# Kernel tuning notes

Measured on AMD Instinct MI355X. Metric: run time of the kernel, lower is better.

The kernel has to match this reference:

```python
import jax, jax.numpy as jnp
import numpy as np
import itertools

N, F, R, O, OUT = 131072, 32, 256, 5, 100
K = 9  # 2*exp_param + 1 with exp_param=4


def setup_inputs() -> dict:
    key = jax.random.key(0)
    k1, k2, k3 = jax.random.split(key, 3)
    # binary features -> get_route(x)==1 -> categorical rule path
    x = jax.random.randint(k1, (N, F), 0, 2).astype(jnp.float32)
    # first R combinations of O feature indices out of F (itertools order, as in __init__)
    combs = np.array(list(itertools.islice(itertools.combinations(range(F), O), R)), dtype=np.int32)
    comb_space = jax.random.normal(k2, (O, R), dtype=jnp.float32)
    w_out = jax.random.normal(k3, (OUT, R), dtype=jnp.float32) * 0.05
    b_out = jnp.zeros((OUT,), jnp.float32)
    return {"x": x, "comb_space": comb_space, "w_out": w_out, "b_out": b_out,
            "comb_idx": jnp.asarray(combs)}


def reference(x, comb_space, w_out, b_out, comb_idx):
    # Fused version of the per-rule Python loop:
    # gather all rule feature subsets at once: [N, R, O]
    gathered = x[:, comb_idx]
    # per-rule dot product with its parameter vector comb_space[:, r]
    scores = jnp.einsum('nro,or->nr', gathered, comb_space)  # [N, R]
    # polyClip activation: clamp(s^k, -1, 1)
    comb_pred = jnp.clip(scores ** K, -1.0, 1.0)
    # dropout p=0.1 is identity in eval mode
    attn = jax.nn.softmax(comb_pred, axis=1)                 # [N, R]
    out = attn @ w_out.T + b_out                             # [N, OUT]
    return jax.nn.log_softmax(out, axis=1)
```

## Files before the change

### kernel.cpp

```cpp
#include <hip/hip_runtime.h>

typedef unsigned short u16;
typedef _Float16 f16;
typedef __attribute__((ext_vector_type(2))) __fp16 hf16x2;
typedef __attribute__((ext_vector_type(4))) _Float16 f16x4;
typedef __attribute__((ext_vector_type(8))) _Float16 f16x8;
typedef __attribute__((ext_vector_type(4))) float f32x4;

#define N_ROWS 131072
#define FDIM 32
#define RDIM 256
#define ODIM 5
#define NOUT 100
#define JT 7
#define WAVES 8
#define ROWS_PER_BLOCK (WAVES * 16)
#define NBLOCKS (N_ROWS / ROWS_PER_BLOCK)

#define MF_SLOTS 1024
#define WF_SLOTS (JT * 8 * 64)
#define TAB_SLOTS (MF_SLOTS + WF_SLOTS)

#define CSCALE 1.04156363f
#define CLIP2  1.44269504f

typedef const __attribute__((address_space(1))) void gvoid;
typedef __attribute__((address_space(3))) void lvoid;

__device__ __forceinline__ u16 f2h_bits(float f) {
    f16 h = (f16)f;
    union { f16 h; u16 u; } v; v.h = h;
    return v.u;
}

__global__ void build_tabs(const float* __restrict__ cs, const float* __restrict__ w,
                           const int* __restrict__ ci, u16* __restrict__ tabs) {
    int t = blockIdx.x * 512 + threadIdx.x;
    if (t >= TAB_SLOTS) return;
    u16 vals[8];
    if (t < MF_SLOTS) {
        int l = t & 63, rt = t >> 6;
        int r = rt * 16 + (l & 15);
        int kbase = (l >> 4) * 8;
        int idx0 = ci[r * ODIM + 0], idx1 = ci[r * ODIM + 1], idx2 = ci[r * ODIM + 2];
        int idx3 = ci[r * ODIM + 3], idx4 = ci[r * ODIM + 4];
#pragma unroll
        for (int e = 0; e < 8; ++e) {
            int k = kbase + e;
            float v = 0.f;
            if (idx0 == k) v = cs[0 * RDIM + r];
            if (idx1 == k) v = cs[1 * RDIM + r];
            if (idx2 == k) v = cs[2 * RDIM + r];
            if (idx3 == k) v = cs[3 * RDIM + r];
            if (idx4 == k) v = cs[4 * RDIM + r];
            vals[e] = f2h_bits(v * CSCALE);
        }
    } else {
        int s = t - MF_SLOTS;
        int l = s & 63, ft = s >> 6;
        int jt = ft >> 3, rtp = ft & 7;
        int j = jt * 16 + (l & 15);
        if (j < NOUT) {
            const float* wp = w + (size_t)j * RDIM + rtp * 32 + (l >> 4) * 4;
            float4 va = *(const float4*)wp;
            float4 vb = *(const float4*)(wp + 16);
            vals[0] = f2h_bits(va.x); vals[1] = f2h_bits(va.y);
            vals[2] = f2h_bits(va.z); vals[3] = f2h_bits(va.w);
            vals[4] = f2h_bits(vb.x); vals[5] = f2h_bits(vb.y);
            vals[6] = f2h_bits(vb.z); vals[7] = f2h_bits(vb.w);
        } else {
            u16 fill = (j == NOUT) ? f2h_bits(1.0f) : (u16)0;
#pragma unroll
            for (int e = 0; e < 8; ++e) vals[e] = fill;
        }
    }
    *(uint4*)(tabs + (size_t)t * 8) = *(const uint4*)vals;
}

__device__ __forceinline__ f16x4 elemop(f32x4 cc) {
    float ev[4];
#pragma unroll
    for (int i = 0; i < 4; ++i) {
        float s = cc[i];
        float s2 = s * s, s4 = s2 * s2, s8 = s4 * s4;
        float p = __builtin_amdgcn_fmed3f(s8 * s, -CLIP2, CLIP2);
        float e;
        asm("v_exp_f32 %0, %1" : "=v"(e) : "v"(p));
        ev[i] = e;
    }
    union { hf16x2 h; unsigned u; } lo, hi;
    lo.h = __builtin_amdgcn_cvt_pkrtz(ev[0], ev[1]);
    hi.h = __builtin_amdgcn_cvt_pkrtz(ev[2], ev[3]);
    union { unsigned u[2]; f16x4 v; } r;
    r.u[0] = lo.u; r.u[1] = hi.u;
    return r.v;
}

__global__ __launch_bounds__(WAVES * 64, 2) void hornet_main(
    const float* __restrict__ x, const u16* __restrict__ tabs,
    const float* __restrict__ b_out, float* __restrict__ out)
{
    __shared__ __align__(16) u16 tab[TAB_SLOTS * 8];

    const int tid = threadIdx.x;
    const int lane = tid & 63;
    const int wid = tid >> 6;
    const int c15 = lane & 15, g = lane >> 4;

    const int rowb0 = blockIdx.x * ROWS_PER_BLOCK + wid * 16;
    const float* xp0 = x + (size_t)(rowb0 + c15) * FDIM + g * 8;
    float4 x0a = ((const float4*)xp0)[0];
    float4 x0b = ((const float4*)xp0)[1];

#pragma unroll
    for (int i = 0; i < 9; ++i) {
        const u16* gp = tabs + (size_t)(tid + i * 512) * 8;
        u16* lp = tab + (size_t)(wid * 64 + i * 512) * 8;
        __builtin_amdgcn_global_load_lds((gvoid*)gp, (lvoid*)lp, 16, 0, 0);
    }

    f16x8 a1;
    a1[0] = (f16)x0a.x; a1[1] = (f16)x0a.y; a1[2] = (f16)x0a.z; a1[3] = (f16)x0a.w;
    a1[4] = (f16)x0b.x; a1[5] = (f16)x0b.y; a1[6] = (f16)x0b.z; a1[7] = (f16)x0b.w;

    __syncthreads();

    const f16x8* mfv = (const f16x8*)tab;
    const f16x8* wfv = (const f16x8*)(tab + MF_SLOTS * 8);

    f32x4 acc[JT];
#pragma unroll
    for (int jt = 0; jt < JT; ++jt) acc[jt] = (f32x4){0.f, 0.f, 0.f, 0.f};

    f16x8 b1a = mfv[lane];
    f16x8 b1b = mfv[64 + lane];

#pragma unroll 1
    for (int rtp = 0; rtp < 8; ++rtp) {
        f16x8 ca = b1a, cb = b1b;
        int nrtp = (rtp + 1) & 7;
        b1a = mfv[(2 * nrtp) * 64 + lane];
        b1b = mfv[(2 * nrtp + 1) * 64 + lane];

        const f32x4 z = {0.f, 0.f, 0.f, 0.f};
        __builtin_amdgcn_s_setprio(1);
        f32x4 cca = __builtin_amdgcn_mfma_f32_16x16x32_f16(ca, a1, z, 0, 0, 0);
        f32x4 ccb = __builtin_amdgcn_mfma_f32_16x16x32_f16(cb, a1, z, 0, 0, 0);
        __builtin_amdgcn_s_setprio(0);

        f16x4 a2lo = elemop(cca);
        f16x4 a2hi = elemop(ccb);

        const f16x8* wrow = wfv + rtp * 64 + lane;
        __builtin_amdgcn_s_setprio(1);
#pragma unroll
        for (int jt = 0; jt < JT; ++jt) {
            f16x8 b2 = wrow[jt * 8 * 64];
            f16x4 b2lo = __builtin_shufflevector(b2, b2, 0, 1, 2, 3);
            f16x4 b2hi = __builtin_shufflevector(b2, b2, 4, 5, 6, 7);
            acc[jt] = __builtin_amdgcn_mfma_f32_16x16x16f16(a2lo, b2lo, acc[jt], 0, 0, 0);
            acc[jt] = __builtin_amdgcn_mfma_f32_16x16x16f16(a2hi, b2hi, acc[jt], 0, 0, 0);
        }
        __builtin_amdgcn_s_setprio(0);
    }

    float bv[JT];
#pragma unroll
    for (int jt = 0; jt < JT; ++jt) {
        int j = jt * 16 + c15;
        bv[jt] = (j < NOUT) ? b_out[j] : 0.f;
    }

    float rin[4];
#pragma unroll
    for (int i = 0; i < 4; ++i)
        rin[i] = __builtin_amdgcn_rcpf(__shfl(acc[6][i], g * 16 + 4, 64));
    const bool v6 = (c15 < 4);
#pragma unroll
    for (int i = 0; i < 4; ++i) {
        float lg[JT];
        float se = 0.f;
#pragma unroll
        for (int jt = 0; jt < 6; ++jt) {
            lg[jt] = fmaf(acc[jt][i], rin[i], bv[jt]);
            se += __expf(lg[jt]);
        }
        lg[6] = fmaf(acc[6][i], rin[i], bv[6]);
        se += v6 ? __expf(lg[6]) : 0.f;
#pragma unroll
        for (int m = 1; m <= 8; m <<= 1) se += __shfl_xor(se, m, 64);
        float lse = __logf(se);
        int row = rowb0 + g * 4 + i;
        float* op = out + (size_t)row * NOUT;
#pragma unroll
        for (int jt = 0; jt < 6; ++jt) op[jt * 16 + c15] = lg[jt] - lse;
        if (v6) op[96 + c15] = lg[6] - lse;
    }
}

extern "C" void kernel_launch(void* const* d_in, const int* in_sizes, int n_in,
                              void* d_out, int out_size, void* d_ws, size_t ws_size,
                              hipStream_t stream) {
    const float* x  = (const float*)d_in[0];
    const float* cs = (const float*)d_in[1];
    const float* w  = (const float*)d_in[2];
    const float* b  = (const float*)d_in[3];
    const int*   ci = (const int*)d_in[4];

    u16* tabs = (u16*)d_ws;

    hipLaunchKernelGGL(build_tabs, dim3(9), dim3(512), 0, stream, cs, w, ci, tabs);
    hipLaunchKernelGGL(hornet_main, dim3(NBLOCKS), dim3(WAVES * 64), 0, stream,
                       x, tabs, b, (float*)d_out);
}
```

Baseline: 31.76 us.

## Read weight tables from global cache, shrink blocks, packed fp16 activation math

Removes the per-block LDS staging of the 72KB weight/mapping tables and reads them directly from global memory (relying on L1/L2 caching). The block shrinks to 4 waves with occupancy target 8. The pow9/clip/exp activation is rewritten as packed fp16 ops with v_exp_f16 instead of fp32 per-element math. This avoids the LDS fill and barrier and the LDS capacity limit on occupancy, at the cost of more global/cache traffic per MFMA operand load and reduced precision in the activation (fp16 overflow of s^9 is clipped).

```diff
diff --git a/kernel.cpp b/kernel.cpp
--- a/kernel.cpp
+++ b/kernel.cpp
@@ -1,6 +1,7 @@
 #include <hip/hip_runtime.h>
 
 typedef unsigned short u16;
+typedef unsigned int u32;
 typedef _Float16 f16;
 typedef __attribute__((ext_vector_type(2))) __fp16 hf16x2;
 typedef __attribute__((ext_vector_type(4))) _Float16 f16x4;
@@ -13,7 +14,7 @@
 #define ODIM 5
 #define NOUT 100
 #define JT 7
-#define WAVES 8
+#define WAVES 4
 #define ROWS_PER_BLOCK (WAVES * 16)
 #define NBLOCKS (N_ROWS / ROWS_PER_BLOCK)
 
@@ -22,10 +23,6 @@
 #define TAB_SLOTS (MF_SLOTS + WF_SLOTS)
 
 #define CSCALE 1.04156363f
-#define CLIP2  1.44269504f
-
-typedef const __attribute__((address_space(1))) void gvoid;
-typedef __attribute__((address_space(3))) void lvoid;
 
 __device__ __forceinline__ u16 f2h_bits(float f) {
     f16 h = (f16)f;
@@ -35,7 +32,7 @@
 
 __global__ void build_tabs(const float* __restrict__ cs, const float* __restrict__ w,
                            const int* __restrict__ ci, u16* __restrict__ tabs) {
-    int t = blockIdx.x * 512 + threadIdx.x;
+    int t = blockIdx.x * 256 + threadIdx.x;
     if (t >= TAB_SLOTS) return;
     u16 vals[8];
     if (t < MF_SLOTS) {
@@ -77,31 +74,35 @@
     *(uint4*)(tabs + (size_t)t * 8) = *(const uint4*)vals;
 }
 
-__device__ __forceinline__ f16x4 elemop(f32x4 cc) {
-    float ev[4];
-#pragma unroll
-    for (int i = 0; i < 4; ++i) {
-        float s = cc[i];
-        float s2 = s * s, s4 = s2 * s2, s8 = s4 * s4;
-        float p = __builtin_amdgcn_fmed3f(s8 * s, -CLIP2, CLIP2);
-        float e;
-        asm("v_exp_f32 %0, %1" : "=v"(e) : "v"(p));
-        ev[i] = e;
-    }
-    union { hf16x2 h; unsigned u; } lo, hi;
-    lo.h = __builtin_amdgcn_cvt_pkrtz(ev[0], ev[1]);
-    hi.h = __builtin_amdgcn_cvt_pkrtz(ev[2], ev[3]);
-    union { unsigned u[2]; f16x4 v; } r;
-    r.u[0] = lo.u; r.u[1] = hi.u;
+__device__ __forceinline__ u32 pk_pow9_clip_exp(u32 h, u32 cpos, u32 cneg, u32 psel) {
+    u32 h2, h4, h8, p, phi, elo, ehi, r;
+    asm("v_pk_mul_f16 %0, %1, %1" : "=v"(h2) : "v"(h));
+    asm("v_pk_mul_f16 %0, %1, %1" : "=v"(h4) : "v"(h2));
+    asm("v_pk_mul_f16 %0, %1, %1" : "=v"(h8) : "v"(h4));
+    asm("v_pk_mul_f16 %0, %1, %2" : "=v"(p) : "v"(h8), "v"(h));
+    asm("v_pk_max_f16 %0, %1, %2" : "=v"(p) : "v"(p), "v"(cneg));
+    asm("v_pk_min_f16 %0, %1, %2" : "=v"(p) : "v"(p), "v"(cpos));
+    asm("v_lshrrev_b32 %0, 16, %1" : "=v"(phi) : "v"(p));
+    asm("v_exp_f16 %0, %1" : "=v"(elo) : "v"(p));
+    asm("v_exp_f16 %0, %1" : "=v"(ehi) : "v"(phi));
+    asm("v_perm_b32 %0, %1, %2, %3" : "=v"(r) : "v"(ehi), "v"(elo), "v"(psel));
+    return r;
+}
+
+__device__ __forceinline__ f16x4 elemop(f32x4 cc, u32 cpos, u32 cneg, u32 psel) {
+    union { hf16x2 h; u32 u; } h01, h23;
+    h01.h = __builtin_amdgcn_cvt_pkrtz(cc[0], cc[1]);
+    h23.h = __builtin_amdgcn_cvt_pkrtz(cc[2], cc[3]);
+    union { u32 u[2]; f16x4 v; } r;
+    r.u[0] = pk_pow9_clip_exp(h01.u, cpos, cneg, psel);
+    r.u[1] = pk_pow9_clip_exp(h23.u, cpos, cneg, psel);
     return r.v;
 }
 
-__global__ __launch_bounds__(WAVES * 64, 2) void hornet_main(
+__global__ __launch_bounds__(WAVES * 64, 8) void hornet_main(
     const float* __restrict__ x, const u16* __restrict__ tabs,
     const float* __restrict__ b_out, float* __restrict__ out)
 {
-    __shared__ __align__(16) u16 tab[TAB_SLOTS * 8];
-
     const int tid = threadIdx.x;
     const int lane = tid & 63;
     const int wid = tid >> 6;
@@ -112,21 +113,16 @@
     float4 x0a = ((const float4*)xp0)[0];
     float4 x0b = ((const float4*)xp0)[1];
 
-#pragma unroll
-    for (int i = 0; i < 9; ++i) {
-        const u16* gp = tabs + (size_t)(tid + i * 512) * 8;
-        u16* lp = tab + (size_t)(wid * 64 + i * 512) * 8;
-        __builtin_amdgcn_global_load_lds((gvoid*)gp, (lvoid*)lp, 16, 0, 0);
-    }
-
     f16x8 a1;
     a1[0] = (f16)x0a.x; a1[1] = (f16)x0a.y; a1[2] = (f16)x0a.z; a1[3] = (f16)x0a.w;
     a1[4] = (f16)x0b.x; a1[5] = (f16)x0b.y; a1[6] = (f16)x0b.z; a1[7] = (f16)x0b.w;
 
-    __syncthreads();
-
-    const f16x8* mfv = (const f16x8*)tab;
-    const f16x8* wfv = (const f16x8*)(tab + MF_SLOTS * 8);
+    const u32 cpos = 0x3DC53DC5u;
+    const u32 cneg = 0xBDC5BDC5u;
+    const u32 psel = 0x05040100u;
+
+    const f16x8* mfv = (const f16x8*)tabs;
+    const f16x8* wfv = (const f16x8*)tabs + MF_SLOTS;
 
     f32x4 acc[JT];
 #pragma unroll
@@ -148,8 +144,8 @@
         f32x4 ccb = __builtin_amdgcn_mfma_f32_16x16x32_f16(cb, a1, z, 0, 0, 0);
         __builtin_amdgcn_s_setprio(0);
 
-        f16x4 a2lo = elemop(cca);
-        f16x4 a2hi = elemop(ccb);
+        f16x4 a2lo = elemop(cca, cpos, cneg, psel);
+        f16x4 a2hi = elemop(ccb, cpos, cneg, psel);
 
         const f16x8* wrow = wfv + rtp * 64 + lane;
         __builtin_amdgcn_s_setprio(1);
@@ -209,7 +205,7 @@
 
     u16* tabs = (u16*)d_ws;
 
-    hipLaunchKernelGGL(build_tabs, dim3(9), dim3(512), 0, stream, cs, w, ci, tabs);
+    hipLaunchKernelGGL(build_tabs, dim3(18), dim3(256), 0, stream, cs, w, ci, tabs);
     hipLaunchKernelGGL(hornet_main, dim3(NBLOCKS), dim3(WAVES * 64), 0, stream,
                        x, tabs, b, (float*)d_out);
 }
```

New measurement: 40.79 us. 28.4% more time.
